# Kernel tuning notes

Hardware: AMD Instinct MI355X
Metric: run time of the kernel (lower is better)

The kernel has to match this reference:

```python
import jax, jax.numpy as jnp
import numpy as np

ARAP_WEIGHT = 1.0


def _decoder(code, W1, b1, W2, b2, W3, b3):
    # code: [D] -> vertices [N, 3]
    h = jax.nn.relu(code @ W1 + b1)
    h = jax.nn.relu(h @ W2 + b2)
    v = h @ W3 + b3
    return v.reshape(-1, 3)


def _arap_per_vertex(xyz1, recon, nbr, num_nbr, wmat):
    # xyz1, recon: [N,3]; nbr: [N,K] int; num_nbr: [N]; wmat: [N,K]
    N, K = nbr.shape
    mask = (jnp.arange(K)[None, :] < num_nbr[:, None]).astype(wmat.dtype)
    w = wmat * mask                              # zero out padded neighbors
    e_rest = xyz1[nbr] - xyz1[:, None, :]        # [N,K,3] rest-pose edges (gather)
    e_def = recon[nbr] - recon[:, None, :]       # [N,K,3] deformed edges (gather)
    # weighted covariance per vertex: S_i = sum_k w_ik e_ik e'_ik^T  -> [N,3,3]
    S = jnp.einsum('nk,nka,nkb->nab', w, e_rest, e_def)
    U, _, Vt = jnp.linalg.svd(S)
    V = jnp.swapaxes(Vt, -1, -2)
    R0 = jnp.einsum('nab,ncb->nac', V, U)        # V U^T
    d = jnp.linalg.det(R0)                       # reflection fix
    diag = jnp.stack([jnp.ones_like(d), jnp.ones_like(d), d], axis=-1)  # [N,3]
    R = jnp.einsum('nab,nb,ncb->nac', V, diag, U)
    R = jax.lax.stop_gradient(R)                 # local-global: rotations fixed in bwd
    e_rot = jnp.einsum('nab,nkb->nka', R, e_rest)
    resid = e_def - e_rot
    return jnp.sum(w * jnp.sum(resid * resid, axis=-1), axis=-1)  # [N]


def setup_inputs() -> dict:
    key = jax.random.key(0)
    ks = jax.random.split(key, 12)
    N, K, D = 20000, 16, 256
    H1, H2 = 512, 1024
    inp = {
        'code': jax.random.normal(ks[0], (D,), jnp.float32),
        'xyz1': jax.random.normal(ks[1], (N, 3), jnp.float32),
        'weightMatrix': jax.random.uniform(ks[2], (N, K), jnp.float32),
        'W1': jax.random.normal(ks[3], (D, H1), jnp.float32) * (1.0 / np.sqrt(D)),
        'b1': jax.random.normal(ks[4], (H1,), jnp.float32) * 0.01,
        'W2': jax.random.normal(ks[5], (H1, H2), jnp.float32) * (1.0 / np.sqrt(H1)),
        'b2': jax.random.normal(ks[6], (H2,), jnp.float32) * 0.01,
        'W3': jax.random.normal(ks[7], (H2, N * 3), jnp.float32) * (1.0 / np.sqrt(H2)),
        'b3': jax.random.normal(ks[8], (N * 3,), jnp.float32) * 0.01,
        'neighborsMatrix': jax.random.randint(ks[9], (N, K), 0, N, jnp.int64),
        'numNeighbors': jax.random.randint(ks[10], (N,), 0, 17, jnp.int64),
    }
    return inp


def reference(code, xyz1, weightMatrix, W1, b1, W2, b2, W3, b3,
              neighborsMatrix, numNeighbors):
    def energy(c):
        recon = _decoder(c, W1, b1, W2, b2, W3, b3)
        pv = _arap_per_vertex(xyz1, recon, neighborsMatrix, numNeighbors, weightMatrix)
        return ARAP_WEIGHT * jnp.mean(pv)

    E, g = jax.value_and_grad(energy)(code)
    # torch module returns (arapEnergy.item(), -code.grad) with arapEnergy = -E
    return (-E, g)
```

## Files before the change

kernel.cpp:

```cpp
#include <hip/hip_runtime.h>
#include <hip/hip_bf16.h>

#define N_V   20000
#define KNB   16
#define DCODE 256
#define H1    512
#define H2    1024
#define M3    60000

#define OFF_L1P   0
#define OFF_L2P   4096
#define OFF_VPART 12288
#define OFF_V     492288
#define OFF_GV    552288
#define OFF_GZ2   612288
#define OFF_GZ1   613312
#define OFF_H1    613824
#define OFF_H2    614336
#define OFF_HC    615360
#define OFF_LIST  616384
#define OFF_CNT   617408
#define OFF_E     617410
#define OFF_R     617412


__global__ void k_l1p(const float* __restrict__ code, const float* __restrict__ W1,
                      float* __restrict__ ws) {
    int m = blockIdx.x * 256 + threadIdx.x;
    int d0 = blockIdx.y * 32;
    float acc = 0.f;
#pragma unroll
    for (int d = 0; d < 32; ++d)
        acc += code[d0 + d] * W1[(size_t)(d0 + d) * H1 + m];
    ws[OFF_L1P + blockIdx.y * H1 + m] = acc;
    int gid = (blockIdx.y * 2 + blockIdx.x) * 256 + threadIdx.x;
    for (int idx = gid; idx < M3; idx += 4096) ws[OFF_GV + idx] = 0.f;
    if (gid == 0) { ws[OFF_E] = 0.f; ws[OFF_E + 1] = 0.f; }
}

__global__ void k_l2p(const float* __restrict__ b1, const float* __restrict__ W2,
                      float* __restrict__ ws) {
    __shared__ float h1s[64];
    int dz = blockIdx.y, d0 = dz * 64;
    int t = threadIdx.x;
    if (t < 64) {
        float s = b1[d0 + t];
#pragma unroll
        for (int p = 0; p < 8; ++p) s += ws[OFF_L1P + p * H1 + d0 + t];
        float h = fmaxf(s, 0.f);
        h1s[t] = h;
        if (blockIdx.x == 0) ws[OFF_H1 + d0 + t] = h;
    }
    __syncthreads();
    int m = blockIdx.x * 256 + t;
    float acc = 0.f;
#pragma unroll 8
    for (int d = 0; d < 64; ++d)
        acc += h1s[d] * W2[(size_t)(d0 + d) * H2 + m];
    ws[OFF_L2P + dz * H2 + m] = acc;
}

__global__ void k_compact(const float* __restrict__ b2, float* __restrict__ ws) {
    __shared__ int scan[256];
    int t = threadIdx.x;
    float h[4]; int c = 0;
#pragma unroll
    for (int q = 0; q < 4; ++q) {
        int j = t * 4 + q;
        float s = b2[j];
#pragma unroll
        for (int p = 0; p < 8; ++p) s += ws[OFF_L2P + p * H2 + j];
        float hv = fmaxf(s, 0.f);
        ws[OFF_H2 + j] = hv;
        ws[OFF_GZ2 + j] = 0.f;
        h[q] = hv;
        c += (hv > 0.f) ? 1 : 0;
    }
    scan[t] = c;
    __syncthreads();
    for (int off = 1; off < 256; off <<= 1) {
        int x = (t >= off) ? scan[t - off] : 0;
        __syncthreads();
        scan[t] += x;
        __syncthreads();
    }
    int base = scan[t] - c;
    int* list = reinterpret_cast<int*>(&ws[OFF_LIST]);
#pragma unroll
    for (int q = 0; q < 4; ++q) {
        if (h[q] > 0.f) {
            list[base] = t * 4 + q;
            ws[OFF_HC + base] = h[q];
            ++base;
        }
    }
    if (t == 255) *reinterpret_cast<int*>(&ws[OFF_CNT]) = scan[255];
}

__global__ void k_l3p(const float* __restrict__ W3, float* __restrict__ ws) {
    __shared__ int   rlist[128];
    __shared__ float rh[128];
    int jz = blockIdx.y;
    int cnt = *reinterpret_cast<const int*>(&ws[OFF_CNT]);
    int per = (cnt + 7) >> 3;
    int s0 = jz * per;
    int s1 = s0 + per; if (s1 > cnt) s1 = cnt;
    int n = s1 - s0;
    int t = threadIdx.x;
    if (t < 128 && t < n) {
        rlist[t] = reinterpret_cast<const int*>(&ws[OFF_LIST])[s0 + t];
        rh[t]    = ws[OFF_HC + s0 + t];
    }
    __syncthreads();
    int m4 = blockIdx.x * 1024 + t * 4;
    if (m4 >= M3) return;
    float ax = 0.f, ay = 0.f, az = 0.f, aw = 0.f;
    int ii = 0;
    for (; ii + 3 < n; ii += 4) {
        int r0 = rlist[ii], r1 = rlist[ii + 1], r2 = rlist[ii + 2], r3 = rlist[ii + 3];
        float h0 = rh[ii], h1v = rh[ii + 1], h2v = rh[ii + 2], h3 = rh[ii + 3];
        float4 w0 = *reinterpret_cast<const float4*>(&W3[(size_t)r0 * M3 + m4]);
        float4 w1 = *reinterpret_cast<const float4*>(&W3[(size_t)r1 * M3 + m4]);
        float4 w2 = *reinterpret_cast<const float4*>(&W3[(size_t)r2 * M3 + m4]);
        float4 w3 = *reinterpret_cast<const float4*>(&W3[(size_t)r3 * M3 + m4]);
        ax += h0 * w0.x + h1v * w1.x + h2v * w2.x + h3 * w3.x;
        ay += h0 * w0.y + h1v * w1.y + h2v * w2.y + h3 * w3.y;
        az += h0 * w0.z + h1v * w1.z + h2v * w2.z + h3 * w3.z;
        aw += h0 * w0.w + h1v * w1.w + h2v * w2.w + h3 * w3.w;
    }
    for (; ii < n; ++ii) {
        int r0 = rlist[ii]; float h0 = rh[ii];
        float4 w0 = *reinterpret_cast<const float4*>(&W3[(size_t)r0 * M3 + m4]);
        ax += h0 * w0.x; ay += h0 * w0.y; az += h0 * w0.z; aw += h0 * w0.w;
    }
    float4 acc = make_float4(ax, ay, az, aw);
    *reinterpret_cast<float4*>(&ws[OFF_VPART + jz * M3 + m4]) = acc;
}

__global__ void k_vred(const float* __restrict__ b3, float* __restrict__ ws) {
    int i4 = blockIdx.x * 256 + threadIdx.x;
    if (i4 < M3 / 4) {
        int m = i4 * 4;
        float4 a = *reinterpret_cast<const float4*>(&b3[m]);
#pragma unroll
        for (int jz = 0; jz < 8; ++jz) {
            float4 p = *reinterpret_cast<const float4*>(&ws[OFF_VPART + jz * M3 + m]);
            a.x += p.x; a.y += p.y; a.z += p.z; a.w += p.w;
        }
        *reinterpret_cast<float4*>(&ws[OFF_V + m]) = a;
    }
}


__device__ inline void jrotf(float a[3][3], float v[3][3], int p, int q) {
    float apq = a[p][q];
    if (fabsf(apq) < 1e-30f) return;
    float theta = (a[q][q] - a[p][p]) / (2.0f * apq);
    float t;
    if (fabsf(theta) > 1e18f) t = 0.5f / theta;
    else t = copysignf(1.0f, theta) / (fabsf(theta) + sqrtf(theta * theta + 1.0f));
    float c = 1.0f / sqrtf(t * t + 1.0f);
    float s = t * c;
    float app = a[p][p], aqq = a[q][q];
    a[p][p] = app - t * apq;
    a[q][q] = aqq + t * apq;
    a[p][q] = 0.0f; a[q][p] = 0.0f;
    int r = 3 - p - q;
    float arp = a[r][p], arq = a[r][q];
    a[r][p] = c * arp - s * arq; a[p][r] = a[r][p];
    a[r][q] = s * arp + c * arq; a[q][r] = a[r][q];
#pragma unroll
    for (int k2 = 0; k2 < 3; ++k2) {
        float vkp = v[k2][p], vkq = v[k2][q];
        v[k2][p] = c * vkp - s * vkq;
        v[k2][q] = s * vkp + c * vkq;
    }
}

__device__ void compute_Rf(const float S[3][3], float R[3][3]) {
    float A[3][3], V[3][3];
#pragma unroll
    for (int a = 0; a < 3; ++a)
#pragma unroll
        for (int b = 0; b < 3; ++b) {
            float s = 0.0f;
#pragma unroll
            for (int c = 0; c < 3; ++c) s += S[c][a] * S[c][b];
            A[a][b] = s;
            V[a][b] = (a == b) ? 1.0f : 0.0f;
        }
    for (int sweep = 0; sweep < 15; ++sweep) {
        float off = A[0][1]*A[0][1] + A[0][2]*A[0][2] + A[1][2]*A[1][2];
        float dg  = A[0][0]*A[0][0] + A[1][1]*A[1][1] + A[2][2]*A[2][2];
        if (off <= 1e-12f * (dg + 1e-30f)) break;
        jrotf(A, V, 0, 1); jrotf(A, V, 0, 2); jrotf(A, V, 1, 2);
    }
    int id[3] = {0, 1, 2};
    if (A[id[0]][id[0]] < A[id[1]][id[1]]) { int t = id[0]; id[0] = id[1]; id[1] = t; }
    if (A[id[0]][id[0]] < A[id[2]][id[2]]) { int t = id[0]; id[0] = id[2]; id[2] = t; }
    if (A[id[1]][id[1]] < A[id[2]][id[2]]) { int t = id[1]; id[1] = id[2]; id[2] = t; }
    float v0[3], v1[3], v2[3];
#pragma unroll
    for (int r = 0; r < 3; ++r) {
        v0[r] = V[r][id[0]]; v1[r] = V[r][id[1]]; v2[r] = V[r][id[2]];
    }
    float u0[3], u1[3], u2[3];
#pragma unroll
    for (int a = 0; a < 3; ++a)
        u0[a] = S[a][0]*v0[0] + S[a][1]*v0[1] + S[a][2]*v0[2];
    float n0 = sqrtf(u0[0]*u0[0] + u0[1]*u0[1] + u0[2]*u0[2]);
    if (!(n0 > 1e-20f)) {
#pragma unroll
        for (int a = 0; a < 3; ++a)
#pragma unroll
            for (int c = 0; c < 3; ++c) R[a][c] = (a == c) ? 1.0f : 0.0f;
        return;
    }
#pragma unroll
    for (int a = 0; a < 3; ++a) u0[a] /= n0;
    float t1[3];
#pragma unroll
    for (int a = 0; a < 3; ++a)
        t1[a] = S[a][0]*v1[0] + S[a][1]*v1[1] + S[a][2]*v1[2];
    float dp = u0[0]*t1[0] + u0[1]*t1[1] + u0[2]*t1[2];
#pragma unroll
    for (int a = 0; a < 3; ++a) t1[a] -= dp * u0[a];
    float n1 = sqrtf(t1[0]*t1[0] + t1[1]*t1[1] + t1[2]*t1[2]);
    if (n1 > 1e-5f * n0) {
#pragma unroll
        for (int a = 0; a < 3; ++a) u1[a] = t1[a] / n1;
    } else {
        int m = (fabsf(u0[0]) <= fabsf(u0[1]) && fabsf(u0[0]) <= fabsf(u0[2])) ? 0
              : (fabsf(u0[1]) <= fabsf(u0[2]) ? 1 : 2);
        float e[3] = {0.0f, 0.0f, 0.0f}; e[m] = 1.0f;
        float cx[3] = { u0[1]*e[2] - u0[2]*e[1],
                        u0[2]*e[0] - u0[0]*e[2],
                        u0[0]*e[1] - u0[1]*e[0] };
        float nn = sqrtf(cx[0]*cx[0] + cx[1]*cx[1] + cx[2]*cx[2]);
#pragma unroll
        for (int a = 0; a < 3; ++a) u1[a] = cx[a] / nn;
    }
    u2[0] = u0[1]*u1[2] - u0[2]*u1[1];
    u2[1] = u0[2]*u1[0] - u0[0]*u1[2];
    u2[2] = u0[0]*u1[1] - u0[1]*u1[0];
    float d = v0[0]*(v1[1]*v2[2] - v1[2]*v2[1])
            - v0[1]*(v1[0]*v2[2] - v1[2]*v2[0])
            + v0[2]*(v1[0]*v2[1] - v1[1]*v2[0]);
#pragma unroll
    for (int a = 0; a < 3; ++a)
#pragma unroll
        for (int c = 0; c < 3; ++c)
            R[a][c] = v0[a]*u0[c] + v1[a]*u1[c] + d * (v2[a]*u2[c]);
}

__global__ void k_arapR(const float* __restrict__ xyz1, const float* __restrict__ wmat,
                        const int* __restrict__ nbr, const int* __restrict__ nnum,
                        float* __restrict__ ws) {
    int i = blockIdx.x * 64 + threadIdx.x;
    if (i >= N_V) return;
    const float* recon = ws + OFF_V;
    int num = nnum[i]; if (num > KNB) num = KNB;
    float cr0 = xyz1[3*i], cr1 = xyz1[3*i+1], cr2 = xyz1[3*i+2];
    float cd0 = recon[3*i], cd1 = recon[3*i+1], cd2 = recon[3*i+2];
    float S[3][3] = {{0,0,0},{0,0,0},{0,0,0}};
    for (int k = 0; k < num; ++k) {
        int j = nbr[i*KNB + k];
        float w = wmat[i*KNB + k];
        float er0 = xyz1[3*j]   - cr0, er1 = xyz1[3*j+1] - cr1, er2 = xyz1[3*j+2] - cr2;
        float ed0 = recon[3*j]  - cd0, ed1 = recon[3*j+1] - cd1, ed2 = recon[3*j+2] - cd2;
        S[0][0] += w*er0*ed0; S[0][1] += w*er0*ed1; S[0][2] += w*er0*ed2;
        S[1][0] += w*er1*ed0; S[1][1] += w*er1*ed1; S[1][2] += w*er1*ed2;
        S[2][0] += w*er2*ed0; S[2][1] += w*er2*ed1; S[2][2] += w*er2*ed2;
    }
    float R[3][3];
    compute_Rf(S, R);
#pragma unroll
    for (int a = 0; a < 3; ++a)
#pragma unroll
        for (int c = 0; c < 3; ++c)
            ws[OFF_R + (a*3 + c) * N_V + i] = R[a][c];
}

__global__ void k_arapG(const float* __restrict__ xyz1, const float* __restrict__ wmat,
                        const int* __restrict__ nbr, const int* __restrict__ nnum,
                        float* __restrict__ ws) {
    const float* recon = ws + OFF_V;
    float* gv = ws + OFF_GV;
    int i = blockIdx.x * 64 + threadIdx.x;
    double pv = 0.0;
    if (i < N_V) {
        int num = nnum[i]; if (num > KNB) num = KNB;
        float cr0 = xyz1[3*i], cr1 = xyz1[3*i+1], cr2 = xyz1[3*i+2];
        float cd0 = recon[3*i], cd1 = recon[3*i+1], cd2 = recon[3*i+2];
        float R00 = ws[OFF_R + 0*N_V + i], R01 = ws[OFF_R + 1*N_V + i], R02 = ws[OFF_R + 2*N_V + i];
        float R10 = ws[OFF_R + 3*N_V + i], R11 = ws[OFF_R + 4*N_V + i], R12 = ws[OFF_R + 5*N_V + i];
        float R20 = ws[OFF_R + 6*N_V + i], R21 = ws[OFF_R + 7*N_V + i], R22 = ws[OFF_R + 8*N_V + i];
        const float gscale = 2.0f / (float)N_V;
        float own0 = 0.f, own1 = 0.f, own2 = 0.f;
        for (int k = 0; k < num; ++k) {
            int j = nbr[i*KNB + k];
            float w = wmat[i*KNB + k];
            float er0 = xyz1[3*j]   - cr0, er1 = xyz1[3*j+1] - cr1, er2 = xyz1[3*j+2] - cr2;
            float ed0 = recon[3*j]  - cd0, ed1 = recon[3*j+1] - cd1, ed2 = recon[3*j+2] - cd2;
            float r0 = ed0 - (R00*er0 + R01*er1 + R02*er2);
            float r1 = ed1 - (R10*er0 + R11*er1 + R12*er2);
            float r2 = ed2 - (R20*er0 + R21*er1 + R22*er2);
            pv += (double)(w * (r0*r0 + r1*r1 + r2*r2));
            float g0 = gscale * w * r0;
            float g1 = gscale * w * r1;
            float g2 = gscale * w * r2;
            atomicAdd(&gv[3*j+0], g0);
            atomicAdd(&gv[3*j+1], g1);
            atomicAdd(&gv[3*j+2], g2);
            own0 += g0; own1 += g1; own2 += g2;
        }
        if (num > 0) {
            atomicAdd(&gv[3*i+0], -own0);
            atomicAdd(&gv[3*i+1], -own1);
            atomicAdd(&gv[3*i+2], -own2);
        }
    }
#pragma unroll
    for (int m = 32; m; m >>= 1) pv += __shfl_xor(pv, m);
    if (threadIdx.x == 0)
        atomicAdd(reinterpret_cast<double*>(ws + OFF_E), pv);
}


__global__ void k_gh2(const float* __restrict__ W3, float* __restrict__ ws) {
    int b = blockIdx.x;
    int cnt = *reinterpret_cast<const int*>(&ws[OFF_CNT]);
    if (b >= cnt) return;
    int j = reinterpret_cast<const int*>(&ws[OFF_LIST])[b];
    const float4* w3r = reinterpret_cast<const float4*>(W3 + (size_t)j * M3);
    const float4* gv4 = reinterpret_cast<const float4*>(ws + OFF_GV);
    float acc = 0.f;
    for (int it = threadIdx.x; it < M3 / 4; it += 256) {
        float4 a = w3r[it], g = gv4[it];
        acc += a.x*g.x + a.y*g.y + a.z*g.z + a.w*g.w;
    }
    for (int m = 32; m; m >>= 1) acc += __shfl_xor(acc, m);
    __shared__ float wsum[4];
    if ((threadIdx.x & 63) == 0) wsum[threadIdx.x >> 6] = acc;
    __syncthreads();
    if (threadIdx.x == 0) ws[OFF_GZ2 + j] = wsum[0] + wsum[1] + wsum[2] + wsum[3];
}

__global__ void k_gh1(const float* __restrict__ W2, float* __restrict__ ws) {
    int wv = threadIdx.x >> 6, ln = threadIdx.x & 63;
    int i = blockIdx.x * 4 + wv;
    const float* gz2 = ws + OFF_GZ2;
    float acc = 0.f;
#pragma unroll
    for (int it = 0; it < H2 / 64; ++it) {
        int jj = ln + it * 64;
        acc += W2[(size_t)i * H2 + jj] * gz2[jj];
    }
    for (int m = 32; m; m >>= 1) acc += __shfl_xor(acc, m);
    if (ln == 0) ws[OFF_GZ1 + i] = (ws[OFF_H1 + i] > 0.f) ? acc : 0.f;
}

__global__ void k_gcode(const float* __restrict__ W1, float* __restrict__ ws,
                        float* __restrict__ out) {
    int wv = threadIdx.x >> 6, ln = threadIdx.x & 63;
    int d = blockIdx.x * 4 + wv;
    const float* gz1 = ws + OFF_GZ1;
    float acc = 0.f;
#pragma unroll
    for (int it = 0; it < H1 / 64; ++it) {
        int ii = ln + it * 64;
        acc += W1[(size_t)d * H1 + ii] * gz1[ii];
    }
    for (int m = 32; m; m >>= 1) acc += __shfl_xor(acc, m);
    if (ln == 0) out[1 + d] = acc;
    if (blockIdx.x == 0 && threadIdx.x == 0) {
        double E = *reinterpret_cast<const double*>(ws + OFF_E);
        out[0] = (float)(-(E / (double)N_V));
    }
}

extern "C" void kernel_launch(void* const* d_in, const int* in_sizes, int n_in,
                              void* d_out, int out_size, void* d_ws, size_t ws_size,
                              hipStream_t stream) {
    const float* code = (const float*)d_in[0];
    const float* xyz1 = (const float*)d_in[1];
    const float* wmat = (const float*)d_in[2];
    const float* W1   = (const float*)d_in[3];
    const float* b1   = (const float*)d_in[4];
    const float* W2   = (const float*)d_in[5];
    const float* b2   = (const float*)d_in[6];
    const float* W3   = (const float*)d_in[7];
    const float* b3   = (const float*)d_in[8];
    const int*   nbr  = (const int*)d_in[9];
    const int*   nnum = (const int*)d_in[10];
    float* out = (float*)d_out;
    float* ws  = (float*)d_ws;

    k_l1p    <<<dim3(2, 8),  256, 0, stream>>>(code, W1, ws);
    k_l2p    <<<dim3(4, 8),  256, 0, stream>>>(b1, W2, ws);
    k_compact<<<1,           256, 0, stream>>>(b2, ws);
    k_l3p    <<<dim3(59, 8), 256, 0, stream>>>(W3, ws);
    k_vred   <<<59,          256, 0, stream>>>(b3, ws);
    k_arapR  <<<313,          64, 0, stream>>>(xyz1, wmat, nbr, nnum, ws);
    k_arapG  <<<313,          64, 0, stream>>>(xyz1, wmat, nbr, nnum, ws);
    k_gh2    <<<1024,        256, 0, stream>>>(W3, ws);
    k_gh1    <<<128,         256, 0, stream>>>(W2, ws);
    k_gcode  <<<64,          256, 0, stream>>>(W1, ws, out);
}
```

Measured before the change: 120.9 us.

## Fuse MLP layers 1-2, merge ARAP kernels, pair rows in gh2, unroll l3p

Merges the first two decoder layers into one kernel, with each block recomputing its 64 hidden units of layer 1. Fuses the ARAP rotation and gradient kernels so neighbour data is gathered once, held in registers, and the R round trip through memory disappears. k_gh2 now handles two W3 rows per block so each gv load is shared, and k_l3p issues 8 loads per iteration instead of 4. The tradeoffs are higher register pressure in the fused ARAP kernel (16x7 floats per thread, running at 79 blocks) and redundant layer-1 work.

After: 120.8 us. No clear change (-0.1%).

```diff
diff --git a/kernel.cpp b/kernel.cpp
--- a/kernel.cpp
+++ b/kernel.cpp
@@ -8,56 +8,55 @@
 #define H2    1024
 #define M3    60000
 
-#define OFF_L1P   0
-#define OFF_L2P   4096
-#define OFF_VPART 12288
-#define OFF_V     492288
-#define OFF_GV    552288
-#define OFF_GZ2   612288
-#define OFF_GZ1   613312
-#define OFF_H1    613824
-#define OFF_H2    614336
-#define OFF_HC    615360
-#define OFF_LIST  616384
-#define OFF_CNT   617408
-#define OFF_E     617410
-#define OFF_R     617412
-
-
-__global__ void k_l1p(const float* __restrict__ code, const float* __restrict__ W1,
-                      float* __restrict__ ws) {
-    int m = blockIdx.x * 256 + threadIdx.x;
-    int d0 = blockIdx.y * 32;
-    float acc = 0.f;
-#pragma unroll
-    for (int d = 0; d < 32; ++d)
-        acc += code[d0 + d] * W1[(size_t)(d0 + d) * H1 + m];
-    ws[OFF_L1P + blockIdx.y * H1 + m] = acc;
-    int gid = (blockIdx.y * 2 + blockIdx.x) * 256 + threadIdx.x;
-    for (int idx = gid; idx < M3; idx += 4096) ws[OFF_GV + idx] = 0.f;
-    if (gid == 0) { ws[OFF_E] = 0.f; ws[OFF_E + 1] = 0.f; }
-}
-
-__global__ void k_l2p(const float* __restrict__ b1, const float* __restrict__ W2,
-                      float* __restrict__ ws) {
+#define OFF_L2P   0
+#define OFF_VPART 8192
+#define OFF_V     488192
+#define OFF_GV    548192
+#define OFF_GZ2   608192
+#define OFF_GZ1   609216
+#define OFF_H1    609728
+#define OFF_H2    610240
+#define OFF_HC    611264
+#define OFF_LIST  612288
+#define OFF_CNT   613312
+#define OFF_E     613316
+
+__global__ void k_mlp12(const float* __restrict__ code, const float* __restrict__ W1,
+                        const float* __restrict__ b1, const float* __restrict__ W2,
+                        float* __restrict__ ws) {
+    __shared__ float red[4][64];
     __shared__ float h1s[64];
-    int dz = blockIdx.y, d0 = dz * 64;
     int t = threadIdx.x;
-    if (t < 64) {
-        float s = b1[d0 + t];
-#pragma unroll
-        for (int p = 0; p < 8; ++p) s += ws[OFF_L1P + p * H1 + d0 + t];
-        float h = fmaxf(s, 0.f);
-        h1s[t] = h;
-        if (blockIdx.x == 0) ws[OFF_H1 + d0 + t] = h;
-    }
-    __syncthreads();
-    int m = blockIdx.x * 256 + t;
+    int bx = blockIdx.x, dz = blockIdx.y;
+    int d0 = dz * 64;
+
+    int ln = t & 63, g = t >> 6;
+    {
+        float acc = 0.f;
+        int r0 = g * 64;
+#pragma unroll 8
+        for (int rr = 0; rr < 64; ++rr)
+            acc += code[r0 + rr] * W1[(size_t)(r0 + rr) * H1 + d0 + ln];
+        red[g][ln] = acc;
+    }
+    __syncthreads();
+    if (g == 0) {
+        float h = fmaxf(red[0][ln] + red[1][ln] + red[2][ln] + red[3][ln] + b1[d0 + ln], 0.f);
+        h1s[ln] = h;
+        if (bx == 0) ws[OFF_H1 + d0 + ln] = h;
+    }
+    __syncthreads();
+
+    int m = bx * 256 + t;
     float acc = 0.f;
 #pragma unroll 8
-    for (int d = 0; d < 64; ++d)
-        acc += h1s[d] * W2[(size_t)(d0 + d) * H2 + m];
+    for (int dd = 0; dd < 64; ++dd)
+        acc += h1s[dd] * W2[(size_t)(d0 + dd) * H2 + m];
     ws[OFF_L2P + dz * H2 + m] = acc;
+
+    int gid = (dz * 4 + bx) * 256 + t;
+    for (int idx = gid; idx < M3; idx += 8192) ws[OFF_GV + idx] = 0.f;
+    if (gid == 0) { ws[OFF_E] = 0.f; ws[OFF_E + 1] = 0.f; }
 }
 
 __global__ void k_compact(const float* __restrict__ b2, float* __restrict__ ws) {
@@ -116,25 +115,24 @@
     if (m4 >= M3) return;
     float ax = 0.f, ay = 0.f, az = 0.f, aw = 0.f;
     int ii = 0;
-    for (; ii + 3 < n; ii += 4) {
-        int r0 = rlist[ii], r1 = rlist[ii + 1], r2 = rlist[ii + 2], r3 = rlist[ii + 3];
-        float h0 = rh[ii], h1v = rh[ii + 1], h2v = rh[ii + 2], h3 = rh[ii + 3];
-        float4 w0 = *reinterpret_cast<const float4*>(&W3[(size_t)r0 * M3 + m4]);
-        float4 w1 = *reinterpret_cast<const float4*>(&W3[(size_t)r1 * M3 + m4]);
-        float4 w2 = *reinterpret_cast<const float4*>(&W3[(size_t)r2 * M3 + m4]);
-        float4 w3 = *reinterpret_cast<const float4*>(&W3[(size_t)r3 * M3 + m4]);
-        ax += h0 * w0.x + h1v * w1.x + h2v * w2.x + h3 * w3.x;
-        ay += h0 * w0.y + h1v * w1.y + h2v * w2.y + h3 * w3.y;
-        az += h0 * w0.z + h1v * w1.z + h2v * w2.z + h3 * w3.z;
-        aw += h0 * w0.w + h1v * w1.w + h2v * w2.w + h3 * w3.w;
+    for (; ii + 7 < n; ii += 8) {
+        float4 wv[8];
+#pragma unroll
+        for (int u = 0; u < 8; ++u)
+            wv[u] = *reinterpret_cast<const float4*>(&W3[(size_t)rlist[ii + u] * M3 + m4]);
+#pragma unroll
+        for (int u = 0; u < 8; ++u) {
+            float h = rh[ii + u];
+            ax += h * wv[u].x; ay += h * wv[u].y; az += h * wv[u].z; aw += h * wv[u].w;
+        }
     }
     for (; ii < n; ++ii) {
-        int r0 = rlist[ii]; float h0 = rh[ii];
-        float4 w0 = *reinterpret_cast<const float4*>(&W3[(size_t)r0 * M3 + m4]);
-        ax += h0 * w0.x; ay += h0 * w0.y; az += h0 * w0.z; aw += h0 * w0.w;
-    }
-    float4 acc = make_float4(ax, ay, az, aw);
-    *reinterpret_cast<float4*>(&ws[OFF_VPART + jz * M3 + m4]) = acc;
+        float h = rh[ii];
+        float4 wv = *reinterpret_cast<const float4*>(&W3[(size_t)rlist[ii] * M3 + m4]);
+        ax += h * wv.x; ay += h * wv.y; az += h * wv.z; aw += h * wv.w;
+    }
+    *reinterpret_cast<float4*>(&ws[OFF_VPART + jz * M3 + m4]) =
+        make_float4(ax, ay, az, aw);
 }
 
 __global__ void k_vred(const float* __restrict__ b3, float* __restrict__ ws) {
@@ -253,66 +251,55 @@
             R[a][c] = v0[a]*u0[c] + v1[a]*u1[c] + d * (v2[a]*u2[c]);
 }
 
-__global__ void k_arapR(const float* __restrict__ xyz1, const float* __restrict__ wmat,
-                        const int* __restrict__ nbr, const int* __restrict__ nnum,
-                        float* __restrict__ ws) {
-    int i = blockIdx.x * 64 + threadIdx.x;
-    if (i >= N_V) return;
-    const float* recon = ws + OFF_V;
-    int num = nnum[i]; if (num > KNB) num = KNB;
-    float cr0 = xyz1[3*i], cr1 = xyz1[3*i+1], cr2 = xyz1[3*i+2];
-    float cd0 = recon[3*i], cd1 = recon[3*i+1], cd2 = recon[3*i+2];
-    float S[3][3] = {{0,0,0},{0,0,0},{0,0,0}};
-    for (int k = 0; k < num; ++k) {
-        int j = nbr[i*KNB + k];
-        float w = wmat[i*KNB + k];
-        float er0 = xyz1[3*j]   - cr0, er1 = xyz1[3*j+1] - cr1, er2 = xyz1[3*j+2] - cr2;
-        float ed0 = recon[3*j]  - cd0, ed1 = recon[3*j+1] - cd1, ed2 = recon[3*j+2] - cd2;
-        S[0][0] += w*er0*ed0; S[0][1] += w*er0*ed1; S[0][2] += w*er0*ed2;
-        S[1][0] += w*er1*ed0; S[1][1] += w*er1*ed1; S[1][2] += w*er1*ed2;
-        S[2][0] += w*er2*ed0; S[2][1] += w*er2*ed1; S[2][2] += w*er2*ed2;
-    }
-    float R[3][3];
-    compute_Rf(S, R);
-#pragma unroll
-    for (int a = 0; a < 3; ++a)
-#pragma unroll
-        for (int c = 0; c < 3; ++c)
-            ws[OFF_R + (a*3 + c) * N_V + i] = R[a][c];
-}
-
-__global__ void k_arapG(const float* __restrict__ xyz1, const float* __restrict__ wmat,
-                        const int* __restrict__ nbr, const int* __restrict__ nnum,
-                        float* __restrict__ ws) {
+__global__ void k_arap(const float* __restrict__ xyz1, const float* __restrict__ wmat,
+                       const int* __restrict__ nbr, const int* __restrict__ nnum,
+                       float* __restrict__ ws) {
     const float* recon = ws + OFF_V;
     float* gv = ws + OFF_GV;
-    int i = blockIdx.x * 64 + threadIdx.x;
+    int i = blockIdx.x * 256 + threadIdx.x;
     double pv = 0.0;
     if (i < N_V) {
         int num = nnum[i]; if (num > KNB) num = KNB;
         float cr0 = xyz1[3*i], cr1 = xyz1[3*i+1], cr2 = xyz1[3*i+2];
         float cd0 = recon[3*i], cd1 = recon[3*i+1], cd2 = recon[3*i+2];
-        float R00 = ws[OFF_R + 0*N_V + i], R01 = ws[OFF_R + 1*N_V + i], R02 = ws[OFF_R + 2*N_V + i];
-        float R10 = ws[OFF_R + 3*N_V + i], R11 = ws[OFF_R + 4*N_V + i], R12 = ws[OFF_R + 5*N_V + i];
-        float R20 = ws[OFF_R + 6*N_V + i], R21 = ws[OFF_R + 7*N_V + i], R22 = ws[OFF_R + 8*N_V + i];
+        float er[KNB][3], ed[KNB][3], wk[KNB];
+        int   jn[KNB];
+        float S[3][3] = {{0,0,0},{0,0,0},{0,0,0}};
+#pragma unroll
+        for (int k = 0; k < KNB; ++k) {
+            bool live = (k < num);
+            int j = live ? nbr[i*KNB + k] : i;
+            float w = live ? wmat[i*KNB + k] : 0.f;
+            jn[k] = j; wk[k] = w;
+            float e0 = xyz1[3*j]   - cr0, e1 = xyz1[3*j+1] - cr1, e2 = xyz1[3*j+2] - cr2;
+            float f0 = recon[3*j]  - cd0, f1 = recon[3*j+1] - cd1, f2 = recon[3*j+2] - cd2;
+            er[k][0] = e0; er[k][1] = e1; er[k][2] = e2;
+            ed[k][0] = f0; ed[k][1] = f1; ed[k][2] = f2;
+            S[0][0] += w*e0*f0; S[0][1] += w*e0*f1; S[0][2] += w*e0*f2;
+            S[1][0] += w*e1*f0; S[1][1] += w*e1*f1; S[1][2] += w*e1*f2;
+            S[2][0] += w*e2*f0; S[2][1] += w*e2*f1; S[2][2] += w*e2*f2;
+        }
+        float R[3][3];
+        compute_Rf(S, R);
         const float gscale = 2.0f / (float)N_V;
         float own0 = 0.f, own1 = 0.f, own2 = 0.f;
-        for (int k = 0; k < num; ++k) {
-            int j = nbr[i*KNB + k];
-            float w = wmat[i*KNB + k];
-            float er0 = xyz1[3*j]   - cr0, er1 = xyz1[3*j+1] - cr1, er2 = xyz1[3*j+2] - cr2;
-            float ed0 = recon[3*j]  - cd0, ed1 = recon[3*j+1] - cd1, ed2 = recon[3*j+2] - cd2;
-            float r0 = ed0 - (R00*er0 + R01*er1 + R02*er2);
-            float r1 = ed1 - (R10*er0 + R11*er1 + R12*er2);
-            float r2 = ed2 - (R20*er0 + R21*er1 + R22*er2);
-            pv += (double)(w * (r0*r0 + r1*r1 + r2*r2));
-            float g0 = gscale * w * r0;
-            float g1 = gscale * w * r1;
-            float g2 = gscale * w * r2;
-            atomicAdd(&gv[3*j+0], g0);
-            atomicAdd(&gv[3*j+1], g1);
-            atomicAdd(&gv[3*j+2], g2);
-            own0 += g0; own1 += g1; own2 += g2;
+#pragma unroll
+        for (int k = 0; k < KNB; ++k) {
+            if (k < num) {
+                float w = wk[k];
+                float r0 = ed[k][0] - (R[0][0]*er[k][0] + R[0][1]*er[k][1] + R[0][2]*er[k][2]);
+                float r1 = ed[k][1] - (R[1][0]*er[k][0] + R[1][1]*er[k][1] + R[1][2]*er[k][2]);
+                float r2 = ed[k][2] - (R[2][0]*er[k][0] + R[2][1]*er[k][1] + R[2][2]*er[k][2]);
+                pv += (double)(w * (r0*r0 + r1*r1 + r2*r2));
+                float g0 = gscale * w * r0;
+                float g1 = gscale * w * r1;
+                float g2 = gscale * w * r2;
+                int j = jn[k];
+                atomicAdd(&gv[3*j+0], g0);
+                atomicAdd(&gv[3*j+1], g1);
+                atomicAdd(&gv[3*j+2], g2);
+                own0 += g0; own1 += g1; own2 += g2;
+            }
         }
         if (num > 0) {
             atomicAdd(&gv[3*i+0], -own0);
@@ -322,28 +309,49 @@
     }
 #pragma unroll
     for (int m = 32; m; m >>= 1) pv += __shfl_xor(pv, m);
+    __shared__ double wred[4];
+    if ((threadIdx.x & 63) == 0) wred[threadIdx.x >> 6] = pv;
+    __syncthreads();
     if (threadIdx.x == 0)
-        atomicAdd(reinterpret_cast<double*>(ws + OFF_E), pv);
+        atomicAdd(reinterpret_cast<double*>(ws + OFF_E),
+                  wred[0] + wred[1] + wred[2] + wred[3]);
 }
 
 
 __global__ void k_gh2(const float* __restrict__ W3, float* __restrict__ ws) {
     int b = blockIdx.x;
     int cnt = *reinterpret_cast<const int*>(&ws[OFF_CNT]);
-    if (b >= cnt) return;
-    int j = reinterpret_cast<const int*>(&ws[OFF_LIST])[b];
-    const float4* w3r = reinterpret_cast<const float4*>(W3 + (size_t)j * M3);
-    const float4* gv4 = reinterpret_cast<const float4*>(ws + OFF_GV);
-    float acc = 0.f;
+    if (2 * b >= cnt) return;
+    const int* list = reinterpret_cast<const int*>(&ws[OFF_LIST]);
+    int j0 = list[2 * b];
+    bool has1 = (2 * b + 1 < cnt);
+    int j1 = has1 ? list[2 * b + 1] : j0;
+    const float4* w3r0 = reinterpret_cast<const float4*>(W3 + (size_t)j0 * M3);
+    const float4* w3r1 = reinterpret_cast<const float4*>(W3 + (size_t)j1 * M3);
+    const float4* gv4  = reinterpret_cast<const float4*>(ws + OFF_GV);
+    float acc0 = 0.f, acc1 = 0.f;
     for (int it = threadIdx.x; it < M3 / 4; it += 256) {
-        float4 a = w3r[it], g = gv4[it];
-        acc += a.x*g.x + a.y*g.y + a.z*g.z + a.w*g.w;
-    }
-    for (int m = 32; m; m >>= 1) acc += __shfl_xor(acc, m);
-    __shared__ float wsum[4];
-    if ((threadIdx.x & 63) == 0) wsum[threadIdx.x >> 6] = acc;
-    __syncthreads();
-    if (threadIdx.x == 0) ws[OFF_GZ2 + j] = wsum[0] + wsum[1] + wsum[2] + wsum[3];
+        float4 g = gv4[it];
+        float4 a = w3r0[it];
+        float4 c = w3r1[it];
+        acc0 += a.x*g.x + a.y*g.y + a.z*g.z + a.w*g.w;
+        acc1 += c.x*g.x + c.y*g.y + c.z*g.z + c.w*g.w;
+    }
+    for (int m = 32; m; m >>= 1) {
+        acc0 += __shfl_xor(acc0, m);
+        acc1 += __shfl_xor(acc1, m);
+    }
+    __shared__ float wsum[4][2];
+    if ((threadIdx.x & 63) == 0) {
+        wsum[threadIdx.x >> 6][0] = acc0;
+        wsum[threadIdx.x >> 6][1] = acc1;
+    }
+    __syncthreads();
+    if (threadIdx.x == 0) {
+        ws[OFF_GZ2 + j0] = wsum[0][0] + wsum[1][0] + wsum[2][0] + wsum[3][0];
+        if (has1)
+            ws[OFF_GZ2 + j1] = wsum[0][1] + wsum[1][1] + wsum[2][1] + wsum[3][1];
+    }
 }
 
 __global__ void k_gh1(const float* __restrict__ W2, float* __restrict__ ws) {
@@ -396,14 +404,12 @@
     float* out = (float*)d_out;
     float* ws  = (float*)d_ws;
 
-    k_l1p    <<<dim3(2, 8),  256, 0, stream>>>(code, W1, ws);
-    k_l2p    <<<dim3(4, 8),  256, 0, stream>>>(b1, W2, ws);
+    k_mlp12  <<<dim3(4, 8),  256, 0, stream>>>(code, W1, b1, W2, ws);
     k_compact<<<1,           256, 0, stream>>>(b2, ws);
     k_l3p    <<<dim3(59, 8), 256, 0, stream>>>(W3, ws);
     k_vred   <<<59,          256, 0, stream>>>(b3, ws);
-    k_arapR  <<<313,          64, 0, stream>>>(xyz1, wmat, nbr, nnum, ws);
-    k_arapG  <<<313,          64, 0, stream>>>(xyz1, wmat, nbr, nnum, ws);
-    k_gh2    <<<1024,        256, 0, stream>>>(W3, ws);
+    k_arap   <<<79,          256, 0, stream>>>(xyz1, wmat, nbr, nnum, ws);
+    k_gh2    <<<512,         256, 0, stream>>>(W3, ws);
     k_gh1    <<<128,         256, 0, stream>>>(W2, ws);
     k_gcode  <<<64,          256, 0, stream>>>(W1, ws, out);
 }
```
